# Kernel tuning notes

Hardware: AMD Instinct MI355X
Metric: run time of the kernel (lower is better)

Reference implementation:

```python
import math
import jax, jax.numpy as jnp
import numpy as np

CANTOR_DEPTH = 8
CANTOR_TEMPERATURE = 1.0
SEQ_LEN = 4096


def _cantor_positions(depth_max):
    positions = [np.array([0.0, 1.0])]
    for _ in range(1, depth_max):
        prev = positions[-1]
        new = []
        for i in range(len(prev) - 1):
            left = prev[i]
            right = prev[i + 1]
            third = (right - left) / 3.0
            new.append(left)
            new.append(left + third)
        new.append(prev[-1])
        positions.append(np.array(new))
    return positions


def _cantor_indices(seq_len, depth_max):
    # indices[d] = unique sorted long indices of Cantor positions at depth d
    pos = _cantor_positions(depth_max)
    out = []
    for d in range(depth_max):
        idx = np.unique((pos[d] * (seq_len - 1)).astype(np.int64))
        out.append(jnp.asarray(idx))
    return out


# number of depths actually used in the forward loop
_N_DEPTHS = min(CANTOR_DEPTH, int(math.log2(SEQ_LEN)) + 2)
# get_cantor_indices caps depth at cantor_depth - 1 implicitly via list length
CANTOR_IDX = _cantor_indices(SEQ_LEN, CANTOR_DEPTH)


def setup_inputs() -> dict:
    key0 = jax.random.key(0)
    ks = jax.random.split(key0, 4)
    B, S, D = 8, SEQ_LEN, 512
    return {
        "query": jax.random.normal(ks[0], (B, S, D), dtype=jnp.float32),
        "key": jax.random.normal(ks[1], (B, S, D), dtype=jnp.float32),
        "value": jax.random.normal(ks[2], (B, S, D), dtype=jnp.float32),
        "t": jax.random.normal(ks[3], (B,), dtype=jnp.float32),
        "scale_weights": jnp.ones((CANTOR_DEPTH,), dtype=jnp.float32),
        "scale_temperature": jnp.ones((1,), dtype=jnp.float32),
    }


def reference(query, key, value, t, scale_weights, scale_temperature):
    D = key.shape[-1]
    inv_scale = 1.0 / (math.sqrt(D) * CANTOR_TEMPERATURE)
    scale_outputs = []
    for depth in range(_N_DEPTHS):
        idx = CANTOR_IDX[depth]            # static, <= 2^depth + 1 indices
        sk = key[:, idx]                   # [B, Nd, D] gather
        sv = value[:, idx]                 # [B, Nd, D]
        scores = jnp.einsum("bqd,bkd->bqk", query, sk) * inv_scale
        attn = jax.nn.softmax(scores, axis=-1)
        scale_outputs.append(jnp.einsum("bqk,bkd->bqd", attn, sv))
    stacked = jnp.stack(scale_outputs, axis=0)  # [depths, B, Q, D]
    w = jax.nn.softmax(scale_weights[: len(scale_outputs)] / scale_temperature[0])
    out = jnp.sum(stacked * w[:, None, None, None], axis=0)  # [B, Q, D]
    # torch .squeeze(1) is a no-op here since Q != 1
    return out
```

## Files before the change

kernel.cpp:

```cpp
#include <hip/hip_runtime.h>

#define NDEPTH 8
#define NK 129
#define SEQB 4096
#define DIM 512

typedef short bf16x8 __attribute__((ext_vector_type(8)));
typedef float f32x4  __attribute__((ext_vector_type(4)));

struct CTab { int uidx[NK]; int minD[NK]; int count; };

static constexpr CTab make_ctab() {
    CTab T{};
    double pos[NDEPTH][NK] = {}; int cnt[NDEPTH] = {};
    pos[0][0] = 0.0; pos[0][1] = 1.0; cnt[0] = 2;
    for (int d = 1; d < NDEPTH; ++d) {
        const int n = cnt[d - 1]; int m = 0;
        for (int i = 0; i < n - 1; ++i) {
            const double left = pos[d - 1][i], right = pos[d - 1][i + 1];
            const double third = (right - left) / 3.0;
            pos[d][m++] = left; pos[d][m++] = left + third;
        }
        pos[d][m++] = pos[d - 1][n - 1]; cnt[d] = m;
    }
    int idx[NDEPTH][NK] = {}; int icnt[NDEPTH] = {};
    for (int d = 0; d < NDEPTH; ++d) {
        int m = 0;
        for (int i = 0; i < cnt[d]; ++i) {
            const long long v = (long long)(pos[d][i] * 4095.0);
            bool dup = false;
            for (int k = 0; k < m; ++k) if (idx[d][k] == (int)v) dup = true;
            if (!dup) idx[d][m++] = (int)v;
        }
        icnt[d] = m;
    }
    int u[2 * NK] = {}; int un = 0;
    for (int d = 0; d < NDEPTH; ++d)
        for (int i = 0; i < icnt[d]; ++i) {
            const int v = idx[d][i]; bool f = false;
            for (int k = 0; k < un; ++k) if (u[k] == v) f = true;
            if (!f && un < 2 * NK) u[un++] = v;
        }
    for (int i = 1; i < un; ++i) {
        const int key = u[i]; int k = i - 1;
        while (k >= 0 && u[k] > key) { u[k + 1] = u[k]; --k; }
        u[k + 1] = key;
    }
    T.count = un;
    for (int i = 0; i < un && i < NK; ++i) {
        T.uidx[i] = u[i];
        int md = NDEPTH;
        for (int d = 0; d < NDEPTH && md == NDEPTH; ++d)
            for (int k = 0; k < icnt[d]; ++k)
                if (idx[d][k] == u[i]) { md = d; break; }
        T.minD[i] = md;
    }
    return T;
}
static constexpr CTab h_ct = make_ctab();
static_assert(h_ct.count == NK, "cantor union size mismatch");
__device__ __constant__ CTab g_ct = h_ct;

__device__ __forceinline__ short f2bf(float f) {
    union { float f; unsigned u; } v; v.f = f;
    unsigned r = v.u + 0x7fffu + ((v.u >> 16) & 1u);
    return (short)(r >> 16);
}

__device__ __forceinline__ void gl_lds16(const void* g, void* lds) {
    __builtin_amdgcn_global_load_lds(
        (const __attribute__((address_space(1))) unsigned int*)g,
        (__attribute__((address_space(3))) unsigned int*)lds, 16, 0, 0);
}

#define WSK_ELEMS (8 * 144 * 512)

__global__ __launch_bounds__(256) void ufa_prep(
    const float* __restrict__ K, const float* __restrict__ V,
    short* __restrict__ ws)
{
    short* wsK  = ws;
    short* wsVt = ws + WSK_ELEMS;
    if (blockIdx.x < 1152) {
        const int b = blockIdx.x / 144, key = blockIdx.x % 144;
        short* dst = wsK + ((size_t)b * 144 + key) * 512;
        if (key < NK) {
            const float* src = K + ((size_t)b * SEQB + g_ct.uidx[key]) * DIM;
            for (int i = threadIdx.x; i < 512; i += 256) dst[i] = f2bf(src[i]);
        } else {
            for (int i = threadIdx.x; i < 512; i += 256) dst[i] = 0;
        }
    } else {
        __shared__ float tr[64][133];
        const int id = blockIdx.x - 1152;
        const int b = id / 8, dt = id % 8;
        const float* Vb = V + (size_t)b * SEQB * DIM;
        for (int it = 0; it < 33; ++it) {
            const int k = it * 4 + (int)threadIdx.x / 64;
            const int d = (int)threadIdx.x % 64;
            if (k < NK) tr[d][k] = Vb[(size_t)g_ct.uidx[k] * DIM + dt * 64 + d];
        }
        __syncthreads();
        short* dst = wsVt + ((size_t)b * 512 + dt * 64) * 192;
        for (int idx = threadIdx.x; idx < 64 * 192; idx += 256) {
            const int d = idx / 192, k = idx - d * 192;
            dst[(size_t)d * 192 + k] = (k < NK) ? f2bf(tr[d][k]) : (short)0;
        }
    }
}

__global__ __launch_bounds__(256, 2) void ufa_main(
    const float* __restrict__ Q, const short* __restrict__ ws,
    const float* __restrict__ SW, const float* __restrict__ ST,
    float* __restrict__ Out)
{
    __shared__ char smem[50176];
    char*  kv    = smem;
    short* c_lds = (short*)(smem + 24576);

    const short* wsK  = ws;
    const short* wsVt = ws + WSK_ELEMS;

    const int t    = (int)threadIdx.x;
    const int w    = t >> 6;
    const int lane = t & 63;
    const int m    = lane & 15;
    const int quad = lane >> 4;
    const int b    = (int)blockIdx.x >> 6;
    const int q0   = ((int)blockIdx.x & 63) * 64 + w * 16;

    float wgt[NDEPTH];
    {
        const float it = 1.0f / ST[0];
        float mx = -3.0e38f;
        #pragma unroll
        for (int d = 0; d < NDEPTH; ++d) { wgt[d] = SW[d] * it; mx = fmaxf(mx, wgt[d]); }
        float sum = 0.0f;
        #pragma unroll
        for (int d = 0; d < NDEPTH; ++d) { wgt[d] = __expf(wgt[d] - mx); sum += wgt[d]; }
        const float is = 1.0f / sum;
        #pragma unroll
        for (int d = 0; d < NDEPTH; ++d) wgt[d] *= is;
    }

    f32x4 acc[9];
    #pragma unroll
    for (int tt = 0; tt < 9; ++tt) acc[tt] = (f32x4){0.f, 0.f, 0.f, 0.f};

    const float* Qb  = Q + ((size_t)b * SEQB + q0 + m) * DIM;
    const short* wsKb = wsK + (size_t)b * 144 * 512;

    for (int c = 0; c < 8; ++c) {
        for (int g = w; g < 18; g += 4) {
            const int off  = g * 1024 + lane * 16;
            const int row  = off >> 7;
            const int slot = (off >> 4) & 7;
            const int slog = slot ^ (row & 7);
            gl_lds16(wsKb + (size_t)row * 512 + c * 64 + slog * 8, kv + g * 1024);
        }
        bf16x8 aq[2];
        #pragma unroll
        for (int ks = 0; ks < 2; ++ks) {
            const float* qp = Qb + c * 64 + ks * 32 + quad * 8;
            const float4 x = *(const float4*)qp;
            const float4 y = *(const float4*)(qp + 4);
            aq[ks][0] = f2bf(x.x); aq[ks][1] = f2bf(x.y);
            aq[ks][2] = f2bf(x.z); aq[ks][3] = f2bf(x.w);
            aq[ks][4] = f2bf(y.x); aq[ks][5] = f2bf(y.y);
            aq[ks][6] = f2bf(y.z); aq[ks][7] = f2bf(y.w);
        }
        __syncthreads();
        #pragma unroll
        for (int ks = 0; ks < 2; ++ks) {
            #pragma unroll
            for (int tt = 0; tt < 9; ++tt) {
                const int row  = tt * 16 + m;
                const int slog = (ks * 4 + quad) ^ (row & 7);
                const bf16x8 bk = *(const bf16x8*)(kv + row * 128 + slog * 16);
                acc[tt] = __builtin_amdgcn_mfma_f32_16x16x32_bf16(aq[ks], bk, acc[tt], 0, 0, 0);
            }
        }
        __syncthreads();
    }

    const float inv_scale = 0.04419417382415922f;
    int md9[9];
    #pragma unroll
    for (int tt = 0; tt < 9; ++tt) {
        const int j = tt * 16 + m;
        md9[tt] = (j < NK) ? g_ct.minD[j] : NDEPTH;
    }
    float ev[9][4], mxr[4];
    #pragma unroll
    for (int i = 0; i < 4; ++i) mxr[i] = -3.0e38f;
    #pragma unroll
    for (int tt = 0; tt < 9; ++tt) {
        const bool valid = (tt * 16 + m) < NK;
        #pragma unroll
        for (int i = 0; i < 4; ++i) {
            const float s = valid ? acc[tt][i] * inv_scale : -3.0e38f;
            ev[tt][i] = s;
            mxr[i] = fmaxf(mxr[i], s);
        }
    }
    #pragma unroll
    for (int off = 1; off < 16; off <<= 1)
        #pragma unroll
        for (int i = 0; i < 4; ++i) mxr[i] = fmaxf(mxr[i], __shfl_xor(mxr[i], off));

    float P[4][NDEPTH];
    #pragma unroll
    for (int i = 0; i < 4; ++i)
        #pragma unroll
        for (int d = 0; d < NDEPTH; ++d) P[i][d] = 0.0f;
    #pragma unroll
    for (int tt = 0; tt < 9; ++tt) {
        const int md = md9[tt];
        #pragma unroll
        for (int i = 0; i < 4; ++i) {
            const float e = __expf(ev[tt][i] - mxr[i]);
            ev[tt][i] = e;
            #pragma unroll
            for (int d = 0; d < NDEPTH; ++d) P[i][d] += (md == d) ? e : 0.0f;
        }
    }
    #pragma unroll
    for (int off = 1; off < 16; off <<= 1)
        #pragma unroll
        for (int i = 0; i < 4; ++i)
            #pragma unroll
            for (int d = 0; d < NDEPTH; ++d) P[i][d] += __shfl_xor(P[i][d], off);

    float T[4][NDEPTH];
    #pragma unroll
    for (int i = 0; i < 4; ++i) {
        float L = 0.0f, Lc[NDEPTH];
        #pragma unroll
        for (int d = 0; d < NDEPTH; ++d) { L += P[i][d]; Lc[d] = L; }
        float ta = 0.0f;
        #pragma unroll
        for (int d = NDEPTH - 1; d >= 0; --d) { ta += wgt[d] / Lc[d]; T[i][d] = ta; }
    }
    #pragma unroll
    for (int tt = 0; tt < 10; ++tt) {
        const int j = tt * 16 + m;
        #pragma unroll
        for (int i = 0; i < 4; ++i) {
            float cv = 0.0f;
            if (tt < 9 && j < NK) {
                const int md = md9[tt];
                float tv = 0.0f;
                #pragma unroll
                for (int d = 0; d < NDEPTH; ++d) tv = (md == d) ? T[i][d] : tv;
                cv = ev[tt][i] * tv;
            }
            c_lds[(w * 16 + quad * 4 + i) * 200 + j] = f2bf(cv);
        }
    }
    __syncthreads();

    bf16x8 ac[5];
    #pragma unroll
    for (int ks = 0; ks < 5; ++ks)
        ac[ks] = *(const bf16x8*)&c_lds[(w * 16 + m) * 200 + ks * 32 + quad * 8];

    const short* wsVb = wsVt + (size_t)b * 512 * 192;
    float* Ob = Out + ((size_t)b * SEQB + q0) * DIM;

    for (int c2 = 0; c2 < 8; ++c2) {
        __syncthreads();
        for (int g = w; g < 24; g += 4) {
            const int off  = g * 1024 + lane * 16;
            const int row  = off / 384;
            const int rem  = off - row * 384;
            const int slot = rem >> 4;
            const int slog = (slot & ~7) | ((slot & 7) ^ (row & 7));
            gl_lds16(wsVb + (size_t)(c2 * 64 + row) * 192 + slog * 8, kv + g * 1024);
        }
        __syncthreads();
        #pragma unroll
        for (int nt = 0; nt < 4; ++nt) {
            f32x4 o = (f32x4){0.f, 0.f, 0.f, 0.f};
            #pragma unroll
            for (int ks = 0; ks < 5; ++ks) {
                const int row  = nt * 16 + m;
                const int slot = ks * 4 + quad;
                const int slog = (slot & ~7) | ((slot & 7) ^ (row & 7));
                const bf16x8 bv = *(const bf16x8*)(kv + row * 384 + slog * 16);
                o = __builtin_amdgcn_mfma_f32_16x16x32_bf16(ac[ks], bv, o, 0, 0, 0);
            }
            const int n0 = c2 * 64 + nt * 16;
            #pragma unroll
            for (int i = 0; i < 4; ++i)
                Ob[(size_t)(quad * 4 + i) * DIM + n0 + m] = o[i];
        }
    }
}

extern "C" void kernel_launch(void* const* d_in, const int* in_sizes, int n_in,
                              void* d_out, int out_size, void* d_ws, size_t ws_size,
                              hipStream_t stream) {
    const float* Q  = (const float*)d_in[0];
    const float* K  = (const float*)d_in[1];
    const float* V  = (const float*)d_in[2];
    const float* SW = (const float*)d_in[4];
    const float* ST = (const float*)d_in[5];
    float* Out = (float*)d_out;
    short* ws  = (short*)d_ws;

    ufa_prep<<<dim3(1152 + 64), dim3(256), 0, stream>>>(K, V, ws);
    ufa_main<<<dim3(512), dim3(256), 0, stream>>>(Q, ws, SW, ST, Out);
}
```

Measured before the change: 213.5 us.

## Halve main-kernel block size and rebalance prep kernel work split

The main kernel now runs 128-thread blocks covering 32 queries each, launching twice as many blocks with a smaller LDS footprint. The aim is better occupancy and load balance across the CUs. The prep kernel is regrouped so each K block gathers 8 keys, and the V transpose is split into four key sub-ranges with a smaller shared tile, which gives more parallel V blocks and fewer tiny K blocks. The cost is that each block of two waves has to stage the full K/V chunks into LDS, so K/V loads per query double.

```diff
diff --git a/kernel.cpp b/kernel.cpp
--- a/kernel.cpp
+++ b/kernel.cpp
@@ -81,40 +81,43 @@
 {
     short* wsK  = ws;
     short* wsVt = ws + WSK_ELEMS;
-    if (blockIdx.x < 1152) {
-        const int b = blockIdx.x / 144, key = blockIdx.x % 144;
-        short* dst = wsK + ((size_t)b * 144 + key) * 512;
-        if (key < NK) {
-            const float* src = K + ((size_t)b * SEQB + g_ct.uidx[key]) * DIM;
-            for (int i = threadIdx.x; i < 512; i += 256) dst[i] = f2bf(src[i]);
-        } else {
-            for (int i = threadIdx.x; i < 512; i += 256) dst[i] = 0;
+    if (blockIdx.x < 144) {
+        const int b = blockIdx.x / 18, grp = blockIdx.x % 18;
+        const float* Kb = K + (size_t)b * SEQB * DIM;
+        short* dst = wsK + ((size_t)b * 144 + grp * 8) * 512;
+        for (int i = threadIdx.x; i < 8 * 512; i += 256) {
+            const int r8 = i >> 9, col = i & 511;
+            const int key = grp * 8 + r8;
+            dst[i] = (key < NK) ? f2bf(Kb[(size_t)g_ct.uidx[key] * DIM + col]) : (short)0;
         }
     } else {
-        __shared__ float tr[64][133];
-        const int id = blockIdx.x - 1152;
-        const int b = id / 8, dt = id % 8;
+        __shared__ float tr[64 * 49];
+        const int id = blockIdx.x - 144;
+        const int b = id >> 5, rem = id & 31;
+        const int dt = rem >> 2, ksub = rem & 3;
+        const int kbase = ksub * 48;
         const float* Vb = V + (size_t)b * SEQB * DIM;
-        for (int it = 0; it < 33; ++it) {
-            const int k = it * 4 + (int)threadIdx.x / 64;
-            const int d = (int)threadIdx.x % 64;
-            if (k < NK) tr[d][k] = Vb[(size_t)g_ct.uidx[k] * DIM + dt * 64 + d];
-        }
-        __syncthreads();
-        short* dst = wsVt + ((size_t)b * 512 + dt * 64) * 192;
-        for (int idx = threadIdx.x; idx < 64 * 192; idx += 256) {
-            const int d = idx / 192, k = idx - d * 192;
-            dst[(size_t)d * 192 + k] = (k < NK) ? f2bf(tr[d][k]) : (short)0;
-        }
-    }
-}
-
-__global__ __launch_bounds__(256, 2) void ufa_main(
+        for (int idx = threadIdx.x; idx < 48 * 64; idx += 256) {
+            const int kk = idx >> 6, d = idx & 63;
+            const int k = kbase + kk;
+            tr[d * 49 + kk] = (k < NK)
+                ? Vb[(size_t)g_ct.uidx[k] * DIM + dt * 64 + d] : 0.0f;
+        }
+        __syncthreads();
+        short* dst = wsVt + ((size_t)b * 512 + dt * 64) * 192 + kbase;
+        for (int idx = threadIdx.x; idx < 64 * 48; idx += 256) {
+            const int d = idx / 48, kk = idx - d * 48;
+            dst[(size_t)d * 192 + kk] = f2bf(tr[d * 49 + kk]);
+        }
+    }
+}
+
+__global__ __launch_bounds__(128, 2) void ufa_main(
     const float* __restrict__ Q, const short* __restrict__ ws,
     const float* __restrict__ SW, const float* __restrict__ ST,
     float* __restrict__ Out)
 {
-    __shared__ char smem[50176];
+    __shared__ char smem[24576 + 12800];
     char*  kv    = smem;
     short* c_lds = (short*)(smem + 24576);
 
@@ -126,8 +129,8 @@
     const int lane = t & 63;
     const int m    = lane & 15;
     const int quad = lane >> 4;
-    const int b    = (int)blockIdx.x >> 6;
-    const int q0   = ((int)blockIdx.x & 63) * 64 + w * 16;
+    const int b    = (int)blockIdx.x >> 7;
+    const int q0   = ((int)blockIdx.x & 127) * 32 + w * 16;
 
     float wgt[NDEPTH];
     {
@@ -147,11 +150,11 @@
     #pragma unroll
     for (int tt = 0; tt < 9; ++tt) acc[tt] = (f32x4){0.f, 0.f, 0.f, 0.f};
 
-    const float* Qb  = Q + ((size_t)b * SEQB + q0 + m) * DIM;
+    const float* Qb   = Q + ((size_t)b * SEQB + q0 + m) * DIM;
     const short* wsKb = wsK + (size_t)b * 144 * 512;
 
     for (int c = 0; c < 8; ++c) {
-        for (int g = w; g < 18; g += 4) {
+        for (int g = w; g < 18; g += 2) {
             const int off  = g * 1024 + lane * 16;
             const int row  = off >> 7;
             const int slot = (off >> 4) & 7;
@@ -269,7 +272,7 @@
 
     for (int c2 = 0; c2 < 8; ++c2) {
         __syncthreads();
-        for (int g = w; g < 24; g += 4) {
+        for (int g = w; g < 24; g += 2) {
             const int off  = g * 1024 + lane * 16;
             const int row  = off / 384;
             const int rem  = off - row * 384;
@@ -308,6 +311,6 @@
     float* Out = (float*)d_out;
     short* ws  = (short*)d_ws;
 
-    ufa_prep<<<dim3(1152 + 64), dim3(256), 0, stream>>>(K, V, ws);
-    ufa_main<<<dim3(512), dim3(256), 0, stream>>>(Q, ws, SW, ST, Out);
-}
+    ufa_prep<<<dim3(144 + 256), dim3(256), 0, stream>>>(K, V, ws);
+    ufa_main<<<dim3(1024), dim3(128), 0, stream>>>(Q, ws, SW, ST, Out);
+}
```

Result: slower. 219.7 us (+2.9%).
